# Kernel optimization log

Hardware: AMD Instinct MI355X
Metric: run time of the kernel (lower is better)

Reference implementation:

```python
import jax, jax.numpy as jnp
import numpy as np

EMBED_SIZE = 128
SCALE = EMBED_SIZE ** (-0.5)


def setup_inputs() -> dict:
    key = jax.random.key(0)
    kq, kk, kv = jax.random.split(key, 3)
    B, S, E = 16, 2048, EMBED_SIZE
    return {
        "query": jax.random.normal(kq, (B, S, E), dtype=jnp.float32),
        "key": jax.random.normal(kk, (B, S, E), dtype=jnp.float32),
        "value": jax.random.normal(kv, (B, S, E), dtype=jnp.float32),
    }


def reference(query, key, value):
    # scores: [B, S, S] = q @ k^T, scaled by embed_size**-0.5
    scores = jnp.einsum("bqe,bke->bqk", query, key) * SCALE
    probs = jax.nn.softmax(scores, axis=-1)
    # dropout_p = 0.0 -> identity (deterministic reference)
    out = jnp.einsum("bqk,bke->bqe", probs, value)
    return out
```

## Files before the change

kernel.cpp:

```cpp
#include <hip/hip_runtime.h>

#define SEQ 2048
#define EMB 128
#define KT 64
#define QT 64
#define NT 256
#define NITER (SEQ / KT)

typedef __attribute__((ext_vector_type(8))) short short8;
typedef __attribute__((ext_vector_type(4))) short sh4;
typedef __attribute__((ext_vector_type(4))) float floatx4;
typedef __attribute__((ext_vector_type(4))) unsigned short ushort4_t;

#if __has_builtin(__builtin_amdgcn_mfma_f32_16x16x16_bf16)
#define MFMA16(a, b, c) __builtin_amdgcn_mfma_f32_16x16x16_bf16(a, b, c, 0, 0, 0)
#define HAVE_MFMA16 1
#elif __has_builtin(__builtin_amdgcn_mfma_f32_16x16x16bf16_1k)
#define MFMA16(a, b, c) __builtin_amdgcn_mfma_f32_16x16x16bf16_1k(a, b, c, 0, 0, 0)
#define HAVE_MFMA16 1
#else
#define HAVE_MFMA16 0
#endif

__device__ __forceinline__ unsigned short f2bf(float x) {
  union { float f; unsigned u; } c; c.f = x;
  return (unsigned short)((c.u + 0x7fffu + ((c.u >> 16) & 1u)) >> 16);
}
__device__ __forceinline__ unsigned packbf(float a, float b) {
  return (unsigned)f2bf(a) | ((unsigned)f2bf(b) << 16);
}

__global__ void prep_kernel(const float* __restrict__ K, unsigned short* __restrict__ Kb,
                            const float* __restrict__ V, unsigned short* __restrict__ Vtb,
                            int nblkK) {
  const int tid = threadIdx.x;
  if ((int)blockIdx.x < nblkK) {
    int i = blockIdx.x * NT + tid;
    float4 v = ((const float4*)K)[i];
    ((ushort4_t*)Kb)[i] = (ushort4_t){f2bf(v.x), f2bf(v.y), f2bf(v.z), f2bf(v.w)};
    return;
  }
  const int rb = blockIdx.x - nblkK;
  const int s0 = (rb & 31) * 64;
  const int e0 = ((rb >> 5) & 1) * 64;
  const int b  = rb >> 6;
  const float* src = V + (size_t)b * SEQ * EMB;
  unsigned short* dst = Vtb + (size_t)b * EMB * SEQ;
  const int k = (tid & 15) * 4;
  const int e = (tid >> 4) * 4;
  const float* vb = src + (size_t)(s0 + k) * EMB + e0 + e;
  float4 r0 = *(const float4*)(vb);
  float4 r1 = *(const float4*)(vb + EMB);
  float4 r2 = *(const float4*)(vb + 2 * EMB);
  float4 r3 = *(const float4*)(vb + 3 * EMB);
  unsigned short* d0 = dst + (size_t)(e0 + e) * SEQ + s0 + k;
  *(ushort4_t*)(d0)           = (ushort4_t){f2bf(r0.x), f2bf(r1.x), f2bf(r2.x), f2bf(r3.x)};
  *(ushort4_t*)(d0 + SEQ)     = (ushort4_t){f2bf(r0.y), f2bf(r1.y), f2bf(r2.y), f2bf(r3.y)};
  *(ushort4_t*)(d0 + 2 * SEQ) = (ushort4_t){f2bf(r0.z), f2bf(r1.z), f2bf(r2.z), f2bf(r3.z)};
  *(ushort4_t*)(d0 + 3 * SEQ) = (ushort4_t){f2bf(r0.w), f2bf(r1.w), f2bf(r2.w), f2bf(r3.w)};
}

__global__ __launch_bounds__(NT, 2)
void fattn7(const float* __restrict__ Qp, const unsigned short* __restrict__ Kb,
            const unsigned short* __restrict__ Vtb, float* __restrict__ Op) {
  __shared__ __align__(16) unsigned char smem[65536];
  unsigned short* Ks = (unsigned short*)smem;
  unsigned short* Vs = Ks + 2 * KT * EMB;
  float* Ored = (float*)smem;
  float* lred = (float*)(smem + 2 * 32 * 132 * 4);

  const int tid  = threadIdx.x;
  const int lane = tid & 63;
  const int w    = tid >> 6;
  const int n16  = lane & 15, quad = lane >> 4;
  const int wq   = w & 1;
  const int wk   = w >> 1;
  const int b    = blockIdx.y, q0 = blockIdx.x * QT;
  const size_t bo = (size_t)b * SEQ * EMB;

  auto* ks3 = (__attribute__((address_space(3))) unsigned short*)Ks;
  auto* vs3 = (__attribute__((address_space(3))) unsigned short*)Vs;

  const int krw = tid >> 4, kgs = tid & 15;
  const int vrw = tid >> 3, vgs = tid & 7;
  const unsigned short* pK = Kb + bo + (size_t)krw * EMB + (size_t)((kgs ^ (krw & 7)) * 8);
  const unsigned short* pV = Vtb + bo + (size_t)vrw * SEQ + (size_t)((vgs ^ (vrw & 7)) * 8);

  short8 qf[2][4];
#pragma unroll
  for (int nt = 0; nt < 2; ++nt) {
    const float* qr = Qp + bo + (size_t)(q0 + wq * 32 + nt * 16 + n16) * EMB + quad * 8;
#pragma unroll
    for (int e = 0; e < 4; ++e) {
      float4 x = *(const float4*)(qr + e * 32);
      float4 y = *(const float4*)(qr + e * 32 + 4);
      qf[nt][e] = (short8){(short)f2bf(x.x), (short)f2bf(x.y), (short)f2bf(x.z), (short)f2bf(x.w),
                           (short)f2bf(y.x), (short)f2bf(y.y), (short)f2bf(y.z), (short)f2bf(y.w)};
    }
  }

  int koff[4];
#pragma unroll
  for (int e = 0; e < 4; ++e) koff[e] = ((e * 4 + quad) ^ (n16 & 7)) * 8;

  floatx4 o[8][2];
#pragma unroll
  for (int t = 0; t < 8; ++t)
#pragma unroll
    for (int nt = 0; nt < 2; ++nt) o[t][nt] = (floatx4){0.f, 0.f, 0.f, 0.f};
  float lp[2] = {0.f, 0.f};

  const float SCALE = 0.08838834764831845f;
  const float L2E = 1.4426950408889634f;
  const float C1 = SCALE * L2E;

  auto issue = [&](int buf) {
    auto* kb = ks3 + buf * (KT * EMB) + w * 512;
    auto* vb = vs3 + buf * (EMB * KT) + w * 512;
    const unsigned short* gv = pV;
#pragma unroll
    for (int j = 0; j < 4; ++j) {
      __builtin_amdgcn_global_load_lds((const __attribute__((address_space(1))) void*)pK,
                                       (__attribute__((address_space(3))) void*)(kb + j * 2048), 16, 0, 0);
      pK += 2048;
      __builtin_amdgcn_global_load_lds((const __attribute__((address_space(1))) void*)gv,
                                       (__attribute__((address_space(3))) void*)(vb + j * 2048), 16, 0, 0);
      gv += 32 * SEQ;
    }
    pV += KT;
  };

  issue(0);

#if HAVE_MFMA16
  int voff16[2];
#pragma unroll
  for (int mt = 0; mt < 2; ++mt)
    voff16[mt] = (((wk * 4 + mt * 2 + (quad >> 1)) ^ (n16 & 7)) * 8) + (quad & 1) * 4;

  sh4 vstA[8][2], vstB[8][2];
  unsigned pstA[2][2][2], pstB[2][2][2];
#pragma unroll
  for (int t = 0; t < 8; ++t)
#pragma unroll
    for (int mt = 0; mt < 2; ++mt) vstB[t][mt] = (sh4){0, 0, 0, 0};
#pragma unroll
  for (int mt = 0; mt < 2; ++mt)
#pragma unroll
    for (int nt = 0; nt < 2; ++nt) { pstB[mt][nt][0] = 0; pstB[mt][nt][1] = 0; }

#define FA_BODY(CUR, VC, VP, PC, PP)                                                     \
  {                                                                                      \
    floatx4 s[2][2];                                                                     \
    _Pragma("unroll") for (int mt = 0; mt < 2; ++mt)                                     \
      _Pragma("unroll") for (int nt = 0; nt < 2; ++nt)                                   \
        s[mt][nt] = (floatx4){0.f, 0.f, 0.f, 0.f};                                       \
    const unsigned short* kbase = Ks + (CUR) * (KT * EMB);                               \
    __builtin_amdgcn_s_setprio(1);                                                       \
    _Pragma("unroll") for (int e = 0; e < 4; ++e) {                                      \
      _Pragma("unroll") for (int mt = 0; mt < 2; ++mt) {                                 \
        short8 ak = *(const short8*)(kbase + (wk * 32 + mt * 16 + n16) * EMB + koff[e]); \
        s[mt][0] = __builtin_amdgcn_mfma_f32_16x16x32_bf16(ak, qf[0][e], s[mt][0], 0, 0, 0); \
        s[mt][1] = __builtin_amdgcn_mfma_f32_16x16x32_bf16(ak, qf[1][e], s[mt][1], 0, 0, 0); \
      }                                                                                  \
    }                                                                                    \
    const unsigned short* vbase = Vs + (CUR) * (EMB * KT);                               \
    _Pragma("unroll") for (int t = 0; t < 8; ++t)                                        \
      _Pragma("unroll") for (int mt = 0; mt < 2; ++mt)                                   \
        VC[t][mt] = *(const sh4*)(vbase + (t * 16 + n16) * KT + voff16[mt]);             \
    sh4 pb[2][2];                                                                        \
    _Pragma("unroll") for (int mt = 0; mt < 2; ++mt)                                     \
      _Pragma("unroll") for (int nt = 0; nt < 2; ++nt) {                                 \
        union { unsigned u[2]; sh4 v; } cc;                                              \
        cc.u[0] = PP[mt][nt][0];                                                         \
        cc.u[1] = PP[mt][nt][1];                                                         \
        pb[mt][nt] = cc.v;                                                               \
      }                                                                                  \
    _Pragma("unroll") for (int t = 0; t < 8; ++t)                                        \
      _Pragma("unroll") for (int nt = 0; nt < 2; ++nt)                                   \
        _Pragma("unroll") for (int mt = 0; mt < 2; ++mt)                                 \
          o[t][nt] = MFMA16(VP[t][mt], pb[mt][nt], o[t][nt]);                            \
    __builtin_amdgcn_s_setprio(0);                                                       \
    _Pragma("unroll") for (int mt = 0; mt < 2; ++mt)                                     \
      _Pragma("unroll") for (int nt = 0; nt < 2; ++nt) {                                 \
        float p0 = __builtin_amdgcn_exp2f(s[mt][nt][0] * C1);                            \
        float p1 = __builtin_amdgcn_exp2f(s[mt][nt][1] * C1);                            \
        float p2 = __builtin_amdgcn_exp2f(s[mt][nt][2] * C1);                            \
        float p3 = __builtin_amdgcn_exp2f(s[mt][nt][3] * C1);                            \
        lp[nt] += (p0 + p1) + (p2 + p3);                                                 \
        PC[mt][nt][0] = packbf(p0, p1);                                                  \
        PC[mt][nt][1] = packbf(p2, p3);                                                  \
      }                                                                                  \
  }

  for (int it2 = 0; it2 < NITER / 2; ++it2) {
    __syncthreads();
    issue(1);
    FA_BODY(0, vstA, vstB, pstA, pstB)
    __syncthreads();
    if (it2 + 1 < NITER / 2) issue(0);
    FA_BODY(1, vstB, vstA, pstB, pstA)
  }

  {
    sh4 pb[2][2];
#pragma unroll
    for (int mt = 0; mt < 2; ++mt)
#pragma unroll
      for (int nt = 0; nt < 2; ++nt) {
        union { unsigned u[2]; sh4 v; } cc;
        cc.u[0] = pstB[mt][nt][0];
        cc.u[1] = pstB[mt][nt][1];
        pb[mt][nt] = cc.v;
      }
#pragma unroll
    for (int t = 0; t < 8; ++t)
#pragma unroll
      for (int nt = 0; nt < 2; ++nt)
#pragma unroll
        for (int mt = 0; mt < 2; ++mt)
          o[t][nt] = MFMA16(vstB[t][mt], pb[mt][nt], o[t][nt]);
  }
#else
  const int voff = ((wk * 4 + quad) ^ (n16 & 7)) * 8;
  const int L1 = n16 + ((quad & 1) ? 32 : 0);
  const int L2v = L1 + 16;
  const bool hi = quad >= 2;
  short8 vprev8[8];
  short8 bprev[2];
#pragma unroll
  for (int t = 0; t < 8; ++t) vprev8[t] = (short8){0, 0, 0, 0, 0, 0, 0, 0};
  bprev[0] = (short8){0, 0, 0, 0, 0, 0, 0, 0};
  bprev[1] = (short8){0, 0, 0, 0, 0, 0, 0, 0};

  for (int it = 0; it < NITER; ++it) {
    const int cur = it & 1;
    __syncthreads();
    if (it + 1 < NITER) issue(cur ^ 1);
    floatx4 s[2][2];
#pragma unroll
    for (int mt = 0; mt < 2; ++mt)
#pragma unroll
      for (int nt = 0; nt < 2; ++nt) s[mt][nt] = (floatx4){0.f, 0.f, 0.f, 0.f};
    const unsigned short* kbase = Ks + cur * (KT * EMB);
#pragma unroll
    for (int e = 0; e < 4; ++e) {
#pragma unroll
      for (int mt = 0; mt < 2; ++mt) {
        short8 ak = *(const short8*)(kbase + (wk * 32 + mt * 16 + n16) * EMB + koff[e]);
        s[mt][0] = __builtin_amdgcn_mfma_f32_16x16x32_bf16(ak, qf[0][e], s[mt][0], 0, 0, 0);
        s[mt][1] = __builtin_amdgcn_mfma_f32_16x16x32_bf16(ak, qf[1][e], s[mt][1], 0, 0, 0);
      }
    }
    const unsigned short* vbase = Vs + cur * (EMB * KT);
    short8 vcur8[8];
#pragma unroll
    for (int t = 0; t < 8; ++t)
      vcur8[t] = *(const short8*)(vbase + (t * 16 + n16) * KT + voff);
#pragma unroll
    for (int t = 0; t < 8; ++t) {
      o[t][0] = __builtin_amdgcn_mfma_f32_16x16x32_bf16(vprev8[t], bprev[0], o[t][0], 0, 0, 0);
      o[t][1] = __builtin_amdgcn_mfma_f32_16x16x32_bf16(vprev8[t], bprev[1], o[t][1], 0, 0, 0);
    }
    unsigned pf[2][2][2];
#pragma unroll
    for (int mt = 0; mt < 2; ++mt)
#pragma unroll
      for (int nt = 0; nt < 2; ++nt) {
        float p0 = __builtin_amdgcn_exp2f(s[mt][nt][0] * C1);
        float p1 = __builtin_amdgcn_exp2f(s[mt][nt][1] * C1);
        float p2 = __builtin_amdgcn_exp2f(s[mt][nt][2] * C1);
        float p3 = __builtin_amdgcn_exp2f(s[mt][nt][3] * C1);
        lp[nt] += (p0 + p1) + (p2 + p3);
        pf[mt][nt][0] = packbf(p0, p1);
        pf[mt][nt][1] = packbf(p2, p3);
      }
#pragma unroll
    for (int nt = 0; nt < 2; ++nt) {
      unsigned a0 = __shfl(pf[0][nt][0], L1),  b0 = __shfl(pf[1][nt][0], L1);
      unsigned a1 = __shfl(pf[0][nt][1], L1),  b1 = __shfl(pf[1][nt][1], L1);
      unsigned a2 = __shfl(pf[0][nt][0], L2v), b2 = __shfl(pf[1][nt][0], L2v);
      unsigned a3 = __shfl(pf[0][nt][1], L2v), b3 = __shfl(pf[1][nt][1], L2v);
      union { unsigned u[4]; short8 v; } bf;
      bf.u[0] = hi ? b0 : a0;
      bf.u[1] = hi ? b1 : a1;
      bf.u[2] = hi ? b2 : a2;
      bf.u[3] = hi ? b3 : a3;
      bprev[nt] = bf.v;
    }
#pragma unroll
    for (int t = 0; t < 8; ++t) vprev8[t] = vcur8[t];
  }
#pragma unroll
  for (int t = 0; t < 8; ++t) {
    o[t][0] = __builtin_amdgcn_mfma_f32_16x16x32_bf16(vprev8[t], bprev[0], o[t][0], 0, 0, 0);
    o[t][1] = __builtin_amdgcn_mfma_f32_16x16x32_bf16(vprev8[t], bprev[1], o[t][1], 0, 0, 0);
  }
#endif

#pragma unroll
  for (int nt = 0; nt < 2; ++nt) {
    lp[nt] += __shfl_xor(lp[nt], 16);
    lp[nt] += __shfl_xor(lp[nt], 32);
  }
  __syncthreads();
  if (wk) {
#pragma unroll
    for (int t = 0; t < 8; ++t)
#pragma unroll
      for (int nt = 0; nt < 2; ++nt)
        *(floatx4*)&Ored[((wq * 32) + nt * 16 + n16) * 132 + t * 16 + quad * 4] = o[t][nt];
    if (quad == 0) {
      lred[wq * 32 + n16] = lp[0];
      lred[wq * 32 + 16 + n16] = lp[1];
    }
  }
  __syncthreads();
  if (!wk) {
    float inv[2];
#pragma unroll
    for (int nt = 0; nt < 2; ++nt)
      inv[nt] = 1.0f / (lp[nt] + lred[wq * 32 + nt * 16 + n16]);
#pragma unroll
    for (int t = 0; t < 8; ++t)
#pragma unroll
      for (int nt = 0; nt < 2; ++nt) {
        floatx4 r = *(const floatx4*)&Ored[((wq * 32) + nt * 16 + n16) * 132 + t * 16 + quad * 4];
        const int q = q0 + wq * 32 + nt * 16 + n16;
        float4 st = {(o[t][nt][0] + r[0]) * inv[nt], (o[t][nt][1] + r[1]) * inv[nt],
                     (o[t][nt][2] + r[2]) * inv[nt], (o[t][nt][3] + r[3]) * inv[nt]};
        *(float4*)(Op + bo + (size_t)q * EMB + t * 16 + quad * 4) = st;
      }
  }
}

extern "C" void kernel_launch(void* const* d_in, const int* in_sizes, int n_in,
                              void* d_out, int out_size, void* d_ws, size_t ws_size,
                              hipStream_t stream) {
  const float* Q = (const float*)d_in[0];
  const float* K = (const float*)d_in[1];
  const float* V = (const float*)d_in[2];
  float* O = (float*)d_out;
  const int B = in_sizes[0] / (SEQ * EMB);
  const size_t tsz = (size_t)B * SEQ * EMB;

  unsigned short* Kb = (unsigned short*)d_ws;
  unsigned short* Vtb = Kb + tsz;

  const int nblkK = (int)(tsz / 4 / NT);
  const int nblkV = (SEQ / 64) * (EMB / 64) * B;
  prep_kernel<<<nblkK + nblkV, NT, 0, stream>>>(K, Kb, V, Vtb, nblkK);
  fattn7<<<dim3(SEQ / QT, B), NT, 0, stream>>>(Q, Kb, Vtb, O);
}
```

Before: 143.9 us.

## Load V fragments directly from global memory instead of staging through LDS

Removes the LDS staging of the transposed V tile and instead has each lane read its V fragments straight from global memory (through cache) in the MFMA16 path. The fallback path without 16x16x16 MFMA is dropped and replaced by a stub. Shared memory shrinks from 64KB to about 34KB, which could allow more blocks per CU and cuts LDS traffic and async-copy instructions. The cost is scattered 8-byte global loads with long latency, exposed inside the loop and without prefetch across iterations beyond the existing register double-buffering.

```diff
diff --git a/kernel.cpp b/kernel.cpp
--- a/kernel.cpp
+++ b/kernel.cpp
@@ -14,12 +14,10 @@
 
 #if __has_builtin(__builtin_amdgcn_mfma_f32_16x16x16_bf16)
 #define MFMA16(a, b, c) __builtin_amdgcn_mfma_f32_16x16x16_bf16(a, b, c, 0, 0, 0)
-#define HAVE_MFMA16 1
 #elif __has_builtin(__builtin_amdgcn_mfma_f32_16x16x16bf16_1k)
 #define MFMA16(a, b, c) __builtin_amdgcn_mfma_f32_16x16x16bf16_1k(a, b, c, 0, 0, 0)
-#define HAVE_MFMA16 1
 #else
-#define HAVE_MFMA16 0
+__device__ static inline floatx4 MFMA16(sh4, sh4, floatx4 c) { return c; }
 #endif
 
 __device__ __forceinline__ unsigned short f2bf(float x) {
@@ -63,9 +61,8 @@
 __global__ __launch_bounds__(NT, 2)
 void fattn7(const float* __restrict__ Qp, const unsigned short* __restrict__ Kb,
             const unsigned short* __restrict__ Vtb, float* __restrict__ Op) {
-  __shared__ __align__(16) unsigned char smem[65536];
+  __shared__ __align__(16) unsigned char smem[34048];
   unsigned short* Ks = (unsigned short*)smem;
-  unsigned short* Vs = Ks + 2 * KT * EMB;
   float* Ored = (float*)smem;
   float* lred = (float*)(smem + 2 * 32 * 132 * 4);
 
@@ -79,12 +76,11 @@
   const size_t bo = (size_t)b * SEQ * EMB;
 
   auto* ks3 = (__attribute__((address_space(3))) unsigned short*)Ks;
-  auto* vs3 = (__attribute__((address_space(3))) unsigned short*)Vs;
 
   const int krw = tid >> 4, kgs = tid & 15;
-  const int vrw = tid >> 3, vgs = tid & 7;
   const unsigned short* pK = Kb + bo + (size_t)krw * EMB + (size_t)((kgs ^ (krw & 7)) * 8);
-  const unsigned short* pV = Vtb + bo + (size_t)vrw * SEQ + (size_t)((vgs ^ (vrw & 7)) * 8);
+  const unsigned short* pVg = Vtb + bo + (size_t)n16 * SEQ
+                              + (size_t)(wk * 32 + (quad >> 1) * 8 + (quad & 1) * 4);
 
   short8 qf[2][4];
 #pragma unroll
@@ -116,27 +112,15 @@
 
   auto issue = [&](int buf) {
     auto* kb = ks3 + buf * (KT * EMB) + w * 512;
-    auto* vb = vs3 + buf * (EMB * KT) + w * 512;
-    const unsigned short* gv = pV;
 #pragma unroll
     for (int j = 0; j < 4; ++j) {
       __builtin_amdgcn_global_load_lds((const __attribute__((address_space(1))) void*)pK,
                                        (__attribute__((address_space(3))) void*)(kb + j * 2048), 16, 0, 0);
       pK += 2048;
-      __builtin_amdgcn_global_load_lds((const __attribute__((address_space(1))) void*)gv,
-                                       (__attribute__((address_space(3))) void*)(vb + j * 2048), 16, 0, 0);
-      gv += 32 * SEQ;
     }
-    pV += KT;
   };
 
   issue(0);
-
-#if HAVE_MFMA16
-  int voff16[2];
-#pragma unroll
-  for (int mt = 0; mt < 2; ++mt)
-    voff16[mt] = (((wk * 4 + mt * 2 + (quad >> 1)) ^ (n16 & 7)) * 8) + (quad & 1) * 4;
 
   sh4 vstA[8][2], vstB[8][2];
   unsigned pstA[2][2][2], pstB[2][2][2];
@@ -164,10 +148,10 @@
         s[mt][1] = __builtin_amdgcn_mfma_f32_16x16x32_bf16(ak, qf[1][e], s[mt][1], 0, 0, 0); \
       }                                                                                  \
     }                                                                                    \
-    const unsigned short* vbase = Vs + (CUR) * (EMB * KT);                               \
     _Pragma("unroll") for (int t = 0; t < 8; ++t)                                        \
       _Pragma("unroll") for (int mt = 0; mt < 2; ++mt)                                   \
-        VC[t][mt] = *(const sh4*)(vbase + (t * 16 + n16) * KT + voff16[mt]);             \
+        VC[t][mt] = *(const sh4*)(pVg + (size_t)(t * 16) * SEQ + mt * 16);               \
+    pVg += KT;                                                                           \
     sh4 pb[2][2];                                                                        \
     _Pragma("unroll") for (int mt = 0; mt < 2; ++mt)                                     \
       _Pragma("unroll") for (int nt = 0; nt < 2; ++nt) {                                 \
@@ -221,82 +205,6 @@
         for (int mt = 0; mt < 2; ++mt)
           o[t][nt] = MFMA16(vstB[t][mt], pb[mt][nt], o[t][nt]);
   }
-#else
-  const int voff = ((wk * 4 + quad) ^ (n16 & 7)) * 8;
-  const int L1 = n16 + ((quad & 1) ? 32 : 0);
-  const int L2v = L1 + 16;
-  const bool hi = quad >= 2;
-  short8 vprev8[8];
-  short8 bprev[2];
-#pragma unroll
-  for (int t = 0; t < 8; ++t) vprev8[t] = (short8){0, 0, 0, 0, 0, 0, 0, 0};
-  bprev[0] = (short8){0, 0, 0, 0, 0, 0, 0, 0};
-  bprev[1] = (short8){0, 0, 0, 0, 0, 0, 0, 0};
-
-  for (int it = 0; it < NITER; ++it) {
-    const int cur = it & 1;
-    __syncthreads();
-    if (it + 1 < NITER) issue(cur ^ 1);
-    floatx4 s[2][2];
-#pragma unroll
-    for (int mt = 0; mt < 2; ++mt)
-#pragma unroll
-      for (int nt = 0; nt < 2; ++nt) s[mt][nt] = (floatx4){0.f, 0.f, 0.f, 0.f};
-    const unsigned short* kbase = Ks + cur * (KT * EMB);
-#pragma unroll
-    for (int e = 0; e < 4; ++e) {
-#pragma unroll
-      for (int mt = 0; mt < 2; ++mt) {
-        short8 ak = *(const short8*)(kbase + (wk * 32 + mt * 16 + n16) * EMB + koff[e]);
-        s[mt][0] = __builtin_amdgcn_mfma_f32_16x16x32_bf16(ak, qf[0][e], s[mt][0], 0, 0, 0);
-        s[mt][1] = __builtin_amdgcn_mfma_f32_16x16x32_bf16(ak, qf[1][e], s[mt][1], 0, 0, 0);
-      }
-    }
-    const unsigned short* vbase = Vs + cur * (EMB * KT);
-    short8 vcur8[8];
-#pragma unroll
-    for (int t = 0; t < 8; ++t)
-      vcur8[t] = *(const short8*)(vbase + (t * 16 + n16) * KT + voff);
-#pragma unroll
-    for (int t = 0; t < 8; ++t) {
-      o[t][0] = __builtin_amdgcn_mfma_f32_16x16x32_bf16(vprev8[t], bprev[0], o[t][0], 0, 0, 0);
-      o[t][1] = __builtin_amdgcn_mfma_f32_16x16x32_bf16(vprev8[t], bprev[1], o[t][1], 0, 0, 0);
-    }
-    unsigned pf[2][2][2];
-#pragma unroll
-    for (int mt = 0; mt < 2; ++mt)
-#pragma unroll
-      for (int nt = 0; nt < 2; ++nt) {
-        float p0 = __builtin_amdgcn_exp2f(s[mt][nt][0] * C1);
-        float p1 = __builtin_amdgcn_exp2f(s[mt][nt][1] * C1);
-        float p2 = __builtin_amdgcn_exp2f(s[mt][nt][2] * C1);
-        float p3 = __builtin_amdgcn_exp2f(s[mt][nt][3] * C1);
-        lp[nt] += (p0 + p1) + (p2 + p3);
-        pf[mt][nt][0] = packbf(p0, p1);
-        pf[mt][nt][1] = packbf(p2, p3);
-      }
-#pragma unroll
-    for (int nt = 0; nt < 2; ++nt) {
-      unsigned a0 = __shfl(pf[0][nt][0], L1),  b0 = __shfl(pf[1][nt][0], L1);
-      unsigned a1 = __shfl(pf[0][nt][1], L1),  b1 = __shfl(pf[1][nt][1], L1);
-      unsigned a2 = __shfl(pf[0][nt][0], L2v), b2 = __shfl(pf[1][nt][0], L2v);
-      unsigned a3 = __shfl(pf[0][nt][1], L2v), b3 = __shfl(pf[1][nt][1], L2v);
-      union { unsigned u[4]; short8 v; } bf;
-      bf.u[0] = hi ? b0 : a0;
-      bf.u[1] = hi ? b1 : a1;
-      bf.u[2] = hi ? b2 : a2;
-      bf.u[3] = hi ? b3 : a3;
-      bprev[nt] = bf.v;
-    }
-#pragma unroll
-    for (int t = 0; t < 8; ++t) vprev8[t] = vcur8[t];
-  }
-#pragma unroll
-  for (int t = 0; t < 8; ++t) {
-    o[t][0] = __builtin_amdgcn_mfma_f32_16x16x32_bf16(vprev8[t], bprev[0], o[t][0], 0, 0, 0);
-    o[t][1] = __builtin_amdgcn_mfma_f32_16x16x32_bf16(vprev8[t], bprev[1], o[t][1], 0, 0, 0);
-  }
-#endif
 
 #pragma unroll
   for (int nt = 0; nt < 2; ++nt) {
```

Result: slower. 217.9 us (+51.4%).
